# Performance work log

Measured on AMD Instinct MI355X. Metric: run time of the kernel, lower is better.

The kernel has to match this reference:

```python
import jax, jax.numpy as jnp
import numpy as np

NUM_RELATIONS = 4
N_NODES = 20000
N_EDGES = 320000
F_IN = 128
HID = 128
EMB = 128


def _rgcn_conv(x, src, dst, edge_type, edge_weight, W, root, bias):
    """One WeightedRGCNConv layer.
    x: [N, in]; W: [R, in, out]; root: [in, out]; bias: [out].
    Math identical to m = einsum('ei,eio->eo', x[src], W[edge_type]) but computed
    as R grouped matmuls to avoid materializing the [E, in, out] weight copy.
    """
    xj = x[src]  # [E, in] gather
    m = jnp.zeros((xj.shape[0], W.shape[2]), dtype=x.dtype)
    for r in range(W.shape[0]):  # fixed small relation count
        mask = (edge_type == r).astype(x.dtype)[:, None]
        m = m + mask * (xj @ W[r])
    m = m * edge_weight[:, None]
    out = jax.ops.segment_sum(m, dst, num_segments=x.shape[0])  # scatter_add
    return out + x @ root + bias


def setup_inputs() -> dict:
    key = jax.random.key(0)
    ks = jax.random.split(key, 10)
    return {
        "x": jax.random.normal(ks[0], (N_NODES, F_IN), dtype=jnp.float32),
        "edge_index": jax.random.randint(ks[1], (2, N_EDGES), 0, N_NODES, dtype=jnp.int64 if jax.config.jax_enable_x64 else jnp.int32).astype(jnp.int32),
        "edge_type": jax.random.randint(ks[2], (N_EDGES,), 0, NUM_RELATIONS).astype(jnp.int32),
        "edge_weight": jax.random.uniform(ks[3], (N_EDGES,), dtype=jnp.float32),
        "W1": jax.random.normal(ks[4], (NUM_RELATIONS, F_IN, HID), dtype=jnp.float32) * 0.05,
        "root1": jax.random.normal(ks[5], (F_IN, HID), dtype=jnp.float32) * 0.05,
        "b1": jax.random.normal(ks[6], (HID,), dtype=jnp.float32) * 0.05,
        "W2": jax.random.normal(ks[7], (NUM_RELATIONS, HID, EMB), dtype=jnp.float32) * 0.05,
        "root2": jax.random.normal(ks[8], (HID, EMB), dtype=jnp.float32) * 0.05,
        "b2": jax.random.normal(ks[9], (EMB,), dtype=jnp.float32) * 0.05,
    }


def reference(x, edge_index, edge_type, edge_weight, W1, root1, b1, W2, root2, b2):
    src, dst = edge_index[0], edge_index[1]
    # min-max normalize edge weights (as in RGCN.forward)
    ew = (edge_weight - edge_weight.min()) / (edge_weight.max() - edge_weight.min() + 1e-08)
    h = jax.nn.relu(_rgcn_conv(x, src, dst, edge_type, ew, W1, root1, b1))
    h = _rgcn_conv(h, src, dst, edge_type, ew, W2, root2, b2)
    return h
```

## Files before the change

### kernel.cpp

```cpp
#include <hip/hip_runtime.h>

#define NN 20000
#define NE 320000
#define FD 128
#define KTOT 640
#define NSTEP 20

typedef float f32x4 __attribute__((ext_vector_type(4)));
typedef __bf16 bf16x4 __attribute__((ext_vector_type(4)));
typedef __bf16 bf16x8 __attribute__((ext_vector_type(8)));

__device__ __forceinline__ unsigned f2ord(float f) {
  unsigned u = __float_as_uint(f);
  return (u & 0x80000000u) ? ~u : (u | 0x80000000u);
}
__device__ __forceinline__ float ord2f(unsigned u) {
  return (u & 0x80000000u) ? __uint_as_float(u & 0x7FFFFFFFu) : __uint_as_float(~u);
}
__device__ __forceinline__ unsigned pkbf(float a, float b) {
  union { __bf16 h[2]; unsigned u; } p;
  p.h[0] = (__bf16)a; p.h[1] = (__bf16)b; return p.u;
}
__device__ __forceinline__ void gld16(const void* src, void* lds) {
  __builtin_amdgcn_global_load_lds(
      (const unsigned int __attribute__((address_space(1)))*)src,
      (unsigned int __attribute__((address_space(3)))*)lds, 16, 0, 0);
}

__global__ void prep_kernel(unsigned* mm, int* deg,
                            const float* __restrict__ x, unsigned* __restrict__ xb,
                            const float* __restrict__ W1, const float* __restrict__ r1,
                            const float* __restrict__ W2, const float* __restrict__ r2,
                            __bf16* __restrict__ wt1, __bf16* __restrict__ wt2) {
  int i = blockIdx.x * blockDim.x + threadIdx.x;
  if (i == 0) { mm[0] = 0xFFFFFFFFu; mm[1] = 0u; }
  if (i < NN) deg[i] = 0;
  if (i < 2 * FD * KTOT) {
    int which = i / (FD * KTOT);
    int rem = i % (FD * KTOT);
    int n = rem / KTOT, k = rem % KTOT;
    const float* W = which ? W2 : W1;
    const float* rt = which ? r2 : r1;
    float v = (k < 512) ? W[(size_t)k * FD + n] : rt[(size_t)(k - 512) * FD + n];
    (which ? wt2 : wt1)[rem] = (__bf16)v;
  }
  if (i < NN * FD / 4) {
    float4 v = *(const float4*)(x + (size_t)i * 4);
    uint2 p;
    p.x = pkbf(v.x, v.y);
    p.y = pkbf(v.z, v.w);
    *(uint2*)(xb + (size_t)i * 2) = p;
  }
}

__global__ void histmm_kernel(const int* __restrict__ dst, const float* __restrict__ ew,
                              int* deg, unsigned* mm) {
  __shared__ unsigned smn[256], smx[256];
  unsigned lmn = 0xFFFFFFFFu, lmx = 0u;
  for (int i = blockIdx.x * blockDim.x + threadIdx.x; i < NE; i += gridDim.x * blockDim.x) {
    atomicAdd(&deg[dst[i]], 1);
    unsigned o = f2ord(ew[i]);
    lmn = (o < lmn) ? o : lmn;
    lmx = (o > lmx) ? o : lmx;
  }
  smn[threadIdx.x] = lmn; smx[threadIdx.x] = lmx;
  __syncthreads();
  for (int s = 128; s > 0; s >>= 1) {
    if (threadIdx.x < s) {
      unsigned a = smn[threadIdx.x], b = smn[threadIdx.x + s];
      smn[threadIdx.x] = (b < a) ? b : a;
      unsigned c = smx[threadIdx.x], d = smx[threadIdx.x + s];
      smx[threadIdx.x] = (d > c) ? d : c;
    }
    __syncthreads();
  }
  if (threadIdx.x == 0) { atomicMin(&mm[0], smn[0]); atomicMax(&mm[1], smx[0]); }
}

__global__ void scan_kernel(const int* __restrict__ deg, int* offs, int* cursor) {
  __shared__ int part[1024];
  const int CH = (NN + 1023) / 1024;
  int t = threadIdx.x;
  int b = t * CH;
  int e = (b + CH < NN) ? (b + CH) : NN;
  int s = 0;
  for (int i = b; i < e; ++i) s += deg[i];
  part[t] = s;
  __syncthreads();
  for (int off = 1; off < 1024; off <<= 1) {
    int v = part[t];
    int add = (t >= off) ? part[t - off] : 0;
    __syncthreads();
    part[t] = v + add;
    __syncthreads();
  }
  int excl = (t == 0) ? 0 : part[t - 1];
  for (int i = b; i < e; ++i) { offs[i] = excl; cursor[i] = excl; excl += deg[i]; }
  if (t == 1023) offs[NN] = part[1023];
}

__global__ void fill_kernel(const int* __restrict__ src, const int* __restrict__ dst,
                            const int* __restrict__ et, const float* __restrict__ ew,
                            const unsigned* __restrict__ mm, int* cursor,
                            int2* __restrict__ ed, const uint4* __restrict__ xb4) {
  int e = blockIdx.x * blockDim.x + threadIdx.x;
  if (e >= NE) return;
  float mn = ord2f(mm[0]), mx = ord2f(mm[1]);
  float inv = 1.0f / (mx - mn + 1e-8f);
  int d = dst[e];
  int pos = atomicAdd(&cursor[d], 1);
  ed[pos] = make_int2(src[e] | (et[e] << 28), __float_as_int((ew[e] - mn) * inv));
  uint4 wv = xb4[e];
  asm volatile("" :: "v"(wv.x), "v"(wv.y), "v"(wv.z), "v"(wv.w));
}

__global__ void warm_kernel(const uint4* __restrict__ p, int n4) {
  int i = blockIdx.x * blockDim.x + threadIdx.x;
  if (i < n4) {
    uint4 v = p[i];
    asm volatile("" :: "v"(v.x), "v"(v.y), "v"(v.z), "v"(v.w));
  }
}

__global__ __launch_bounds__(256) void aggregate_kernel(
    const unsigned* __restrict__ xb,
    const int* __restrict__ offs, const int2* __restrict__ ed,
    __bf16* __restrict__ g) {
  int node = (int)((blockIdx.x * blockDim.x + threadIdx.x) >> 6);
  int lane = threadIdx.x & 63;
  if (node >= NN) return;
  int beg = offs[node], end = offs[node + 1];
  float a00 = 0.f, a01 = 0.f, a10 = 0.f, a11 = 0.f;
  float a20 = 0.f, a21 = 0.f, a30 = 0.f, a31 = 0.f;

#define LOADP(E, P0, P1)                                                \
  do {                                                                  \
    int zs_ = (E).x & 0x0FFFFFFF;                                       \
    unsigned zu_ = xb[(size_t)zs_ * 64 + lane];                         \
    P0 = __uint_as_float(zu_ << 16);                                    \
    P1 = __uint_as_float(zu_ & 0xFFFF0000u);                            \
  } while (0)
#define ACCP(E, P0, P1)                                                 \
  do {                                                                  \
    float zw_ = __int_as_float((E).y);                                  \
    unsigned zr_ = ((unsigned)(E).x) >> 28;                             \
    float zw0_ = (zr_ == 0) ? zw_ : 0.f;                                \
    float zw1_ = (zr_ == 1) ? zw_ : 0.f;                                \
    float zw2_ = (zr_ == 2) ? zw_ : 0.f;                                \
    float zw3_ = (zr_ == 3) ? zw_ : 0.f;                                \
    a00 += zw0_ * (P0); a01 += zw0_ * (P1);                             \
    a10 += zw1_ * (P0); a11 += zw1_ * (P1);                             \
    a20 += zw2_ * (P0); a21 += zw2_ * (P1);                             \
    a30 += zw3_ * (P0); a31 += zw3_ * (P1);                             \
  } while (0)

  int j = beg;
  for (; j + 4 <= end; j += 4) {
    int2 e0 = ed[j], e1 = ed[j + 1], e2 = ed[j + 2], e3 = ed[j + 3];
    float p00, p01, p10, p11, p20, p21, p30, p31;
    LOADP(e0, p00, p01); LOADP(e1, p10, p11);
    LOADP(e2, p20, p21); LOADP(e3, p30, p31);
    ACCP(e0, p00, p01); ACCP(e1, p10, p11);
    ACCP(e2, p20, p21); ACCP(e3, p30, p31);
  }
  for (; j < end; ++j) {
    int2 e = ed[j];
    float p0, p1;
    LOADP(e, p0, p1);
    ACCP(e, p0, p1);
  }
#undef LOADP
#undef ACCP

  unsigned* g32 = (unsigned*)(g + (size_t)node * KTOT);
  __builtin_nontemporal_store(pkbf(a00, a01), g32 + 0 * 64 + lane);
  __builtin_nontemporal_store(pkbf(a10, a11), g32 + 1 * 64 + lane);
  __builtin_nontemporal_store(pkbf(a20, a21), g32 + 2 * 64 + lane);
  __builtin_nontemporal_store(pkbf(a30, a31), g32 + 3 * 64 + lane);
  __builtin_nontemporal_store(xb[(size_t)node * 64 + lane], g32 + 4 * 64 + lane);
}

template <int OUT_BF16>
__global__ __launch_bounds__(512) void gemm_kernel(
    const __bf16* __restrict__ gA, const __bf16* __restrict__ wt,
    const float* __restrict__ bias, float* __restrict__ outf,
    __bf16* __restrict__ outb) {
  __shared__ __bf16 As[2][64 * 32];
  __shared__ __bf16 Bs[2][128 * 32];
  int tid = threadIdx.x;
  int wave = tid >> 6, lane = tid & 63;
  int wr = wave >> 1, wc = wave & 1;
  int m0 = blockIdx.x * 64;
  int rl = wr * 16 + (lane & 15);
  int kfe = (lane >> 4) * 8;

  unsigned rowpack = 0, colpack[4];
  {
    int arow = tid >> 3, akof = (tid & 7) * 4;
    int bn = tid >> 2, bkof = (tid & 3) * 8;
    bf16x4 v4, one4;
    bf16x8 v8, one8;
#pragma unroll
    for (int i = 0; i < 4; ++i) one4[i] = (__bf16)1.0f;
#pragma unroll
    for (int i = 0; i < 8; ++i) one8[i] = (__bf16)1.0f;
    __bf16 rv = (__bf16)((float)arow * 0.015625f);
#pragma unroll
    for (int i = 0; i < 4; ++i) v4[i] = rv;
    *(bf16x4*)(&As[0][arow * 32 + akof]) = v4;
    *(bf16x8*)(&Bs[0][bn * 32 + bkof]) = one8;
    __syncthreads();
    bf16x8 pa = *(const bf16x8*)(&As[0][rl * 32 + kfe]);
    bf16x8 pb = *(const bf16x8*)(&Bs[0][(wc * 64 + (lane & 15)) * 32 + kfe]);
    f32x4 P1 = __builtin_amdgcn_mfma_f32_16x16x32_bf16(pa, pb, (f32x4){0.f, 0.f, 0.f, 0.f}, 0, 0, 0);
    __syncthreads();
    __bf16 cv = (__bf16)((float)bn * 0.0078125f);
#pragma unroll
    for (int i = 0; i < 8; ++i) v8[i] = cv;
    *(bf16x4*)(&As[0][arow * 32 + akof]) = one4;
    *(bf16x8*)(&Bs[0][bn * 32 + bkof]) = v8;
    __syncthreads();
    bf16x8 pa1 = *(const bf16x8*)(&As[0][rl * 32 + kfe]);
#pragma unroll
    for (int j = 0; j < 4; ++j)
      rowpack |= ((unsigned)(int)(P1[j] * 2.0f + 0.5f)) << (8 * j);
#pragma unroll
    for (int fn = 0; fn < 4; ++fn) {
      bf16x8 pbc = *(const bf16x8*)(&Bs[0][(wc * 64 + fn * 16 + (lane & 15)) * 32 + kfe]);
      f32x4 P2 = __builtin_amdgcn_mfma_f32_16x16x32_bf16(pa1, pbc, (f32x4){0.f, 0.f, 0.f, 0.f}, 0, 0, 0);
      unsigned cp = 0;
#pragma unroll
      for (int j = 0; j < 4; ++j)
        cp |= ((unsigned)(int)(P2[j] * 4.0f + 0.5f)) << (8 * j);
      colpack[fn] = cp;
    }
    __syncthreads();
  }

  f32x4 acc[4];
#pragma unroll
  for (int i = 0; i < 4; ++i) acc[i] = (f32x4){0.f, 0.f, 0.f, 0.f};

  auto stage = [&](int buf, int k0) {
    if (tid < 256) {
      int row = tid >> 2;
      int m = m0 + row;
      if (m >= NN) m = NN - 1;
      gld16(gA + (size_t)m * KTOT + k0 + (tid & 3) * 8, &As[buf][(tid >> 6) * 512]);
    } else {
      int t = tid - 256;
      int wv = t >> 6;
      int r0 = t >> 2;
      gld16(wt + (size_t)r0 * KTOT + k0 + (t & 3) * 8, &Bs[buf][wv * 512]);
      gld16(wt + (size_t)(64 + r0) * KTOT + k0 + (t & 3) * 8, &Bs[buf][2048 + wv * 512]);
    }
  };

  stage(0, 0);
  __syncthreads();
  int cur = 0;
  for (int step = 0; step < NSTEP; ++step) {
    if (step + 1 < NSTEP) stage(cur ^ 1, (step + 1) * 32);
    bf16x8 a = *(const bf16x8*)(&As[cur][rl * 32 + kfe]);
#pragma unroll
    for (int fn = 0; fn < 4; ++fn) {
      bf16x8 b = *(const bf16x8*)(&Bs[cur][(wc * 64 + fn * 16 + (lane & 15)) * 32 + kfe]);
      acc[fn] = __builtin_amdgcn_mfma_f32_16x16x32_bf16(a, b, acc[fn], 0, 0, 0);
    }
    __syncthreads();
    cur ^= 1;
  }

#pragma unroll
  for (int fn = 0; fn < 4; ++fn) {
#pragma unroll
    for (int j = 0; j < 4; ++j) {
      int rloc = (int)((rowpack >> (8 * j)) & 255u);
      int col = (int)((colpack[fn] >> (8 * j)) & 255u);
      int m = m0 + rloc;
      if (m < NN) {
        float v = acc[fn][j] + bias[col];
        if (OUT_BF16) {
          v = fmaxf(v, 0.f);
          outb[(size_t)m * FD + col] = (__bf16)v;
        } else {
          outf[(size_t)m * FD + col] = v;
        }
      }
    }
  }
}

extern "C" void kernel_launch(void* const* d_in, const int* in_sizes, int n_in,
                              void* d_out, int out_size, void* d_ws, size_t ws_size,
                              hipStream_t stream) {
  const float* x  = (const float*)d_in[0];
  const int*   ei = (const int*)d_in[1];
  const int*   et = (const int*)d_in[2];
  const float* ew = (const float*)d_in[3];
  const float* W1 = (const float*)d_in[4];
  const float* r1 = (const float*)d_in[5];
  const float* b1 = (const float*)d_in[6];
  const float* W2 = (const float*)d_in[7];
  const float* r2 = (const float*)d_in[8];
  const float* b2 = (const float*)d_in[9];
  float* out = (float*)d_out;
  const int* src = ei;
  const int* dst = ei + NE;

  char* w = (char*)d_ws;
  size_t o = 0;
  auto take = [&](size_t bytes) -> char* {
    char* p = w + o;
    o += (bytes + 255) & ~(size_t)255;
    return p;
  };
  unsigned* mm  = (unsigned*)take(8);
  int* deg      = (int*)take((size_t)NN * 4);
  int* offs     = (int*)take((size_t)(NN + 1) * 4);
  int* cursor   = (int*)take((size_t)NN * 4);
  int2* ed      = (int2*)take((size_t)(NE + 8) * 8);
  unsigned* xb  = (unsigned*)take((size_t)NN * 64 * 4);
  __bf16* g     = (__bf16*)take((size_t)NN * KTOT * 2);
  __bf16* h1    = (__bf16*)take((size_t)NN * FD * 2);
  __bf16* wt1   = (__bf16*)take((size_t)FD * KTOT * 2);
  __bf16* wt2   = (__bf16*)take((size_t)FD * KTOT * 2);
  (void)ws_size; (void)n_in; (void)in_sizes; (void)out_size;

  hipLaunchKernelGGL(prep_kernel, dim3((NN * FD / 4 + 255) / 256), dim3(256), 0, stream,
                     mm, deg, x, xb, W1, r1, W2, r2, wt1, wt2);
  hipLaunchKernelGGL(histmm_kernel, dim3(512), dim3(256), 0, stream, dst, ew, deg, mm);
  hipLaunchKernelGGL(scan_kernel, dim3(1), dim3(1024), 0, stream, deg, offs, cursor);
  hipLaunchKernelGGL(fill_kernel, dim3((NE + 255) / 256), dim3(256), 0, stream,
                     src, dst, et, ew, mm, cursor, ed, (const uint4*)xb);
  hipLaunchKernelGGL(aggregate_kernel, dim3(NN / 4), dim3(256), 0, stream, xb, offs, ed, g);
  hipLaunchKernelGGL((gemm_kernel<1>), dim3((NN + 63) / 64), dim3(512), 0, stream,
                     g, wt1, b1, (float*)nullptr, h1);
  hipLaunchKernelGGL(warm_kernel, dim3((NN * 64 / 4 + 255) / 256), dim3(256), 0, stream,
                     (const uint4*)h1, NN * 64 / 4);
  hipLaunchKernelGGL(aggregate_kernel, dim3(NN / 4), dim3(256), 0, stream,
                     (const unsigned*)h1, offs, ed, g);
  hipLaunchKernelGGL((gemm_kernel<0>), dim3((NN + 63) / 64), dim3(512), 0, stream,
                     g, wt2, b2, out, (__bf16*)nullptr);
}
```

Baseline: 170.0 us.

## Split node features into two column planes and aggregate per plane

Node features (x in bf16 and h1) are stored as two planes of 64 columns each, and aggregation runs as two passes, one per plane. Each wave handles two edges at once, one per half-wave, and combines the halves with a cross-half shuffle. The goal is to shrink each gather's working set to 128 bytes per row so it fits in cache better, and to double edge-level parallelism. In exchange the edge list is read twice, there are two extra launches, and the shuffle reduction adds work. The fill kernel's warm read of xb is unchanged.

After: 179.8 us. 1.06x slower.

```diff
diff --git a/kernel.cpp b/kernel.cpp
--- a/kernel.cpp
+++ b/kernel.cpp
@@ -46,10 +46,12 @@
   }
   if (i < NN * FD / 4) {
     float4 v = *(const float4*)(x + (size_t)i * 4);
-    uint2 p;
-    p.x = pkbf(v.x, v.y);
-    p.y = pkbf(v.z, v.w);
-    *(uint2*)(xb + (size_t)i * 2) = p;
+    int node = i >> 5, q = i & 31;
+    int p = q >> 4, w2 = (q & 15) * 2;
+    uint2 pk;
+    pk.x = pkbf(v.x, v.y);
+    pk.y = pkbf(v.z, v.w);
+    *(uint2*)(xb + ((size_t)p * NN + node) * 32 + w2) = pk;
   }
 }
 
@@ -122,62 +124,81 @@
   }
 }
 
-__global__ __launch_bounds__(256) void aggregate_kernel(
-    const unsigned* __restrict__ xb,
+template <int P>
+__global__ __launch_bounds__(256) void agg_pass(
+    const unsigned* __restrict__ xplanes,
     const int* __restrict__ offs, const int2* __restrict__ ed,
-    __bf16* __restrict__ g) {
+    unsigned* __restrict__ g) {
   int node = (int)((blockIdx.x * blockDim.x + threadIdx.x) >> 6);
   int lane = threadIdx.x & 63;
   if (node >= NN) return;
+  int h = lane >> 5, ll = lane & 31;
+  const unsigned* xp = xplanes + (size_t)P * NN * 32;
   int beg = offs[node], end = offs[node + 1];
   float a00 = 0.f, a01 = 0.f, a10 = 0.f, a11 = 0.f;
   float a20 = 0.f, a21 = 0.f, a30 = 0.f, a31 = 0.f;
 
-#define LOADP(E, P0, P1)                                                \
-  do {                                                                  \
-    int zs_ = (E).x & 0x0FFFFFFF;                                       \
-    unsigned zu_ = xb[(size_t)zs_ * 64 + lane];                         \
-    P0 = __uint_as_float(zu_ << 16);                                    \
-    P1 = __uint_as_float(zu_ & 0xFFFF0000u);                            \
+#define ACCW(E, U, WV)                                                   \
+  do {                                                                   \
+    float zp0_ = __uint_as_float((U) << 16);                             \
+    float zp1_ = __uint_as_float((U) & 0xFFFF0000u);                     \
+    unsigned zr_ = ((unsigned)(E).x) >> 28;                              \
+    float zw0_ = (zr_ == 0) ? (WV) : 0.f;                                \
+    float zw1_ = (zr_ == 1) ? (WV) : 0.f;                                \
+    float zw2_ = (zr_ == 2) ? (WV) : 0.f;                                \
+    float zw3_ = (zr_ == 3) ? (WV) : 0.f;                                \
+    a00 += zw0_ * zp0_; a01 += zw0_ * zp1_;                              \
+    a10 += zw1_ * zp0_; a11 += zw1_ * zp1_;                              \
+    a20 += zw2_ * zp0_; a21 += zw2_ * zp1_;                              \
+    a30 += zw3_ * zp0_; a31 += zw3_ * zp1_;                              \
   } while (0)
-#define ACCP(E, P0, P1)                                                 \
-  do {                                                                  \
-    float zw_ = __int_as_float((E).y);                                  \
-    unsigned zr_ = ((unsigned)(E).x) >> 28;                             \
-    float zw0_ = (zr_ == 0) ? zw_ : 0.f;                                \
-    float zw1_ = (zr_ == 1) ? zw_ : 0.f;                                \
-    float zw2_ = (zr_ == 2) ? zw_ : 0.f;                                \
-    float zw3_ = (zr_ == 3) ? zw_ : 0.f;                                \
-    a00 += zw0_ * (P0); a01 += zw0_ * (P1);                             \
-    a10 += zw1_ * (P0); a11 += zw1_ * (P1);                             \
-    a20 += zw2_ * (P0); a21 += zw2_ * (P1);                             \
-    a30 += zw3_ * (P0); a31 += zw3_ * (P1);                             \
-  } while (0)
 
   int j = beg;
+  for (; j + 8 <= end; j += 8) {
+    int2 eA = ed[j + h];
+    int2 eB = ed[j + 2 + h];
+    int2 eC = ed[j + 4 + h];
+    int2 eD = ed[j + 6 + h];
+    unsigned uA = xp[(size_t)(eA.x & 0x0FFFFFFF) * 32 + ll];
+    unsigned uB = xp[(size_t)(eB.x & 0x0FFFFFFF) * 32 + ll];
+    unsigned uC = xp[(size_t)(eC.x & 0x0FFFFFFF) * 32 + ll];
+    unsigned uD = xp[(size_t)(eD.x & 0x0FFFFFFF) * 32 + ll];
+    ACCW(eA, uA, __int_as_float(eA.y));
+    ACCW(eB, uB, __int_as_float(eB.y));
+    ACCW(eC, uC, __int_as_float(eC.y));
+    ACCW(eD, uD, __int_as_float(eD.y));
+  }
   for (; j + 4 <= end; j += 4) {
-    int2 e0 = ed[j], e1 = ed[j + 1], e2 = ed[j + 2], e3 = ed[j + 3];
-    float p00, p01, p10, p11, p20, p21, p30, p31;
-    LOADP(e0, p00, p01); LOADP(e1, p10, p11);
-    LOADP(e2, p20, p21); LOADP(e3, p30, p31);
-    ACCP(e0, p00, p01); ACCP(e1, p10, p11);
-    ACCP(e2, p20, p21); ACCP(e3, p30, p31);
-  }
-  for (; j < end; ++j) {
-    int2 e = ed[j];
-    float p0, p1;
-    LOADP(e, p0, p1);
-    ACCP(e, p0, p1);
-  }
-#undef LOADP
-#undef ACCP
-
-  unsigned* g32 = (unsigned*)(g + (size_t)node * KTOT);
-  __builtin_nontemporal_store(pkbf(a00, a01), g32 + 0 * 64 + lane);
-  __builtin_nontemporal_store(pkbf(a10, a11), g32 + 1 * 64 + lane);
-  __builtin_nontemporal_store(pkbf(a20, a21), g32 + 2 * 64 + lane);
-  __builtin_nontemporal_store(pkbf(a30, a31), g32 + 3 * 64 + lane);
-  __builtin_nontemporal_store(xb[(size_t)node * 64 + lane], g32 + 4 * 64 + lane);
+    int2 eA = ed[j + h];
+    int2 eB = ed[j + 2 + h];
+    unsigned uA = xp[(size_t)(eA.x & 0x0FFFFFFF) * 32 + ll];
+    unsigned uB = xp[(size_t)(eB.x & 0x0FFFFFFF) * 32 + ll];
+    ACCW(eA, uA, __int_as_float(eA.y));
+    ACCW(eB, uB, __int_as_float(eB.y));
+  }
+  for (; j < end; j += 2) {
+    int je = j + h;
+    int2 e = ed[(je < end) ? je : (end - 1)];
+    float wv = (je < end) ? __int_as_float(e.y) : 0.f;
+    unsigned u = xp[(size_t)(e.x & 0x0FFFFFFF) * 32 + ll];
+    ACCW(e, u, wv);
+  }
+#undef ACCW
+
+  a00 += __shfl_xor(a00, 32, 64); a01 += __shfl_xor(a01, 32, 64);
+  a10 += __shfl_xor(a10, 32, 64); a11 += __shfl_xor(a11, 32, 64);
+  a20 += __shfl_xor(a20, 32, 64); a21 += __shfl_xor(a21, 32, 64);
+  a30 += __shfl_xor(a30, 32, 64); a31 += __shfl_xor(a31, 32, 64);
+
+  unsigned* row = g + (size_t)node * 320 + P * 32 + ll;
+  if (h == 0) {
+    row[0]   = pkbf(a00, a01);
+    row[64]  = pkbf(a10, a11);
+    row[256] = xp[(size_t)node * 32 + ll];
+  } else {
+    row[128] = pkbf(a20, a21);
+    row[192] = pkbf(a30, a31);
+  }
 }
 
 template <int OUT_BF16>
@@ -282,7 +303,7 @@
         float v = acc[fn][j] + bias[col];
         if (OUT_BF16) {
           v = fmaxf(v, 0.f);
-          outb[(size_t)m * FD + col] = (__bf16)v;
+          outb[((size_t)(col >> 6) * NN + m) * 64 + (col & 63)] = (__bf16)v;
         } else {
           outf[(size_t)m * FD + col] = v;
         }
@@ -333,13 +354,18 @@
   hipLaunchKernelGGL(scan_kernel, dim3(1), dim3(1024), 0, stream, deg, offs, cursor);
   hipLaunchKernelGGL(fill_kernel, dim3((NE + 255) / 256), dim3(256), 0, stream,
                      src, dst, et, ew, mm, cursor, ed, (const uint4*)xb);
-  hipLaunchKernelGGL(aggregate_kernel, dim3(NN / 4), dim3(256), 0, stream, xb, offs, ed, g);
+  hipLaunchKernelGGL((agg_pass<0>), dim3(NN / 4), dim3(256), 0, stream,
+                     xb, offs, ed, (unsigned*)g);
+  hipLaunchKernelGGL((agg_pass<1>), dim3(NN / 4), dim3(256), 0, stream,
+                     xb, offs, ed, (unsigned*)g);
   hipLaunchKernelGGL((gemm_kernel<1>), dim3((NN + 63) / 64), dim3(512), 0, stream,
                      g, wt1, b1, (float*)nullptr, h1);
   hipLaunchKernelGGL(warm_kernel, dim3((NN * 64 / 4 + 255) / 256), dim3(256), 0, stream,
                      (const uint4*)h1, NN * 64 / 4);
-  hipLaunchKernelGGL(aggregate_kernel, dim3(NN / 4), dim3(256), 0, stream,
-                     (const unsigned*)h1, offs, ed, g);
+  hipLaunchKernelGGL((agg_pass<0>), dim3(NN / 4), dim3(256), 0, stream,
+                     (const unsigned*)h1, offs, ed, (unsigned*)g);
+  hipLaunchKernelGGL((agg_pass<1>), dim3(NN / 4), dim3(256), 0, stream,
+                     (const unsigned*)h1, offs, ed, (unsigned*)g);
   hipLaunchKernelGGL((gemm_kernel<0>), dim3((NN + 63) / 64), dim3(512), 0, stream,
                      g, wt2, b2, out, (__bf16*)nullptr);
 }
```
